# Optimization experiments

Measured on AMD Instinct MI355X. Metric: run time of the kernel, lower is better.

## Reference

```python
import jax, jax.numpy as jnp
import numpy as np

N_NODES = 50000
N_EDGES = 800000
IN_DIM = 64
HID_DIM = 64
OUT_DIM = 16
N_RELS = 16
N_BASES = 4


def setup_inputs() -> dict:
    key = jax.random.key(0)
    ks = jax.random.split(key, 11)
    feats = jax.random.normal(ks[0], (N_NODES, IN_DIM), dtype=jnp.float32)
    src = jax.random.randint(ks[1], (N_EDGES,), 0, N_NODES, dtype=jnp.int32)
    dst = jax.random.randint(ks[2], (N_EDGES,), 0, N_NODES, dtype=jnp.int32)
    edge_type = jax.random.randint(ks[3], (N_EDGES,), 0, N_RELS, dtype=jnp.int32)
    edge_norm = jax.random.uniform(ks[4], (N_EDGES,), dtype=jnp.float32)
    # basis-decomposed relation weights: W[r] = sum_b coef[r,b] * bases[b]
    bases1 = jax.random.normal(ks[5], (N_BASES, IN_DIM, HID_DIM), dtype=jnp.float32) * (1.0 / np.sqrt(IN_DIM))
    coef1 = jax.random.normal(ks[6], (N_RELS, N_BASES), dtype=jnp.float32)
    bias1 = jnp.zeros((HID_DIM,), dtype=jnp.float32)
    bases2 = jax.random.normal(ks[7], (N_BASES, HID_DIM, OUT_DIM), dtype=jnp.float32) * (1.0 / np.sqrt(HID_DIM))
    coef2 = jax.random.normal(ks[8], (N_RELS, N_BASES), dtype=jnp.float32)
    bias2 = jnp.zeros((OUT_DIM,), dtype=jnp.float32)
    return {"feats": feats, "src": src, "dst": dst, "edge_type": edge_type,
            "edge_norm": edge_norm, "bases1": bases1, "coef1": coef1, "bias1": bias1,
            "bases2": bases2, "coef2": coef2, "bias2": bias2}


def _rel_graph_conv(x, src, dst, edge_type, edge_norm, bases, coef, bias):
    """One RelGraphConv layer (basis decomposition, low-mem: gather coef, not W)."""
    xs = x[src]                                   # [E, in]  gather source feats
    t = jnp.einsum('ei,bio->ebo', xs, bases)      # [E, B, out] per-basis transform
    c = coef[edge_type]                            # [E, B]   per-edge relation coefs
    msg = jnp.einsum('eb,ebo->eo', c, t)          # [E, out]
    msg = msg * edge_norm[:, None]                # apply edge norm
    h = jax.ops.segment_sum(msg, dst, num_segments=N_NODES)  # scatter-add by dst
    return jax.nn.relu(h + bias)                  # bias + activation (dropout=0, eval)


def reference(feats, src, dst, edge_type, edge_norm, bases1, coef1, bias1, bases2, coef2, bias2):
    h = _rel_graph_conv(feats, src, dst, edge_type, edge_norm, bases1, coef1, bias1)
    h = _rel_graph_conv(h, src, dst, edge_type, edge_norm, bases2, coef2, bias2)
    return h
```

## Files before the change

### kernel.cpp

```cpp
#include <hip/hip_runtime.h>

#define N_NODES 50000
#define N_EDGES 800000

typedef __attribute__((ext_vector_type(8))) short bf16x8;
typedef __attribute__((ext_vector_type(4))) float f32x4;

__device__ __forceinline__ unsigned bf16rne(float x) {
  unsigned u = __float_as_uint(x);
  return (u + 0x7FFFu + ((u >> 16) & 1u)) >> 16;
}
__device__ __forceinline__ unsigned packbf2(float a, float b) {
  return bf16rne(a) | (bf16rne(b) << 16);
}
__device__ __forceinline__ float bflo(unsigned u) { return __uint_as_float(u << 16); }
__device__ __forceinline__ float bfhi(unsigned u) { return __uint_as_float(u & 0xFFFF0000u); }

__global__ __launch_bounds__(256) void k_prep_hist(
    const float4* __restrict__ feats4, uint2* __restrict__ xbf,
    const float* __restrict__ bases1, const float* __restrict__ bases2,
    unsigned short* __restrict__ b1T, unsigned short* __restrict__ b2p,
    const int* __restrict__ dst, int* __restrict__ deg,
    int* __restrict__ rank) {
  if (blockIdx.x < 3125) {
    const int i = blockIdx.x * 256 + threadIdx.x;
    float4 v = feats4[i];
    xbf[i] = make_uint2(packbf2(v.x, v.y), packbf2(v.z, v.w));
    rank[i] = atomicAdd(&deg[dst[i]], 1);
  } else {
    for (int idx = threadIdx.x; idx < 64 * 256; idx += 256) {
      int o = idx >> 8, q = idx & 255;
      b1T[idx] = (unsigned short)bf16rne(bases1[q * 64 + o]);
    }
    for (int idx = threadIdx.x; idx < 64 * 64; idx += 256) {
      int j = idx >> 6, k = idx & 63;
      int o = j >> 2, b = j & 3;
      b2p[idx] = (unsigned short)bf16rne(bases2[b * 1024 + k * 16 + o]);
    }
  }
}

__global__ __launch_bounds__(1024) void k_scan1(const int* __restrict__ deg,
                                                int* __restrict__ rowp,
                                                int* __restrict__ bsum) {
  __shared__ int wsum[16];
  const int tid = threadIdx.x, lane = tid & 63, wid = tid >> 6;
  const int i = blockIdx.x * 1024 + tid;
  int v = (i < N_NODES) ? deg[i] : 0;
  int incl = v;
#pragma unroll
  for (int off = 1; off < 64; off <<= 1) {
    int t = __shfl_up(incl, off, 64);
    if (lane >= off) incl += t;
  }
  if (lane == 63) wsum[wid] = incl;
  __syncthreads();
  if (tid < 16) {
    int wi = wsum[tid];
#pragma unroll
    for (int off = 1; off < 16; off <<= 1) {
      int t = __shfl_up(wi, off, 64);
      if (lane >= off) wi += t;
    }
    wsum[tid] = wi;
  }
  __syncthreads();
  int woff = (wid > 0) ? wsum[wid - 1] : 0;
  int incl_all = incl + woff;
  if (i < N_NODES) rowp[i + 1] = incl_all;
  if (tid == 1023) bsum[blockIdx.x] = incl_all;
}

__global__ __launch_bounds__(1024) void k_scan3(int* __restrict__ rowp,
                                                const int* __restrict__ bsum,
                                                int nblk) {
  __shared__ int s_off;
  const int tid = threadIdx.x;
  if (tid < 64) {
    int v = (tid < nblk && tid < blockIdx.x) ? bsum[tid] : 0;
#pragma unroll
    for (int off = 32; off >= 1; off >>= 1) v += __shfl_down(v, off, 64);
    if (tid == 0) s_off = v;
  }
  __syncthreads();
  const int i = blockIdx.x * 1024 + tid;
  if (i < N_NODES) rowp[i + 1] += s_off;
  if (i == 0) rowp[0] = 0;
}

__global__ __launch_bounds__(256) void k_scatter(
    const int* __restrict__ src, const int* __restrict__ dst,
    const int* __restrict__ ety, const float* __restrict__ enorm,
    const int* __restrict__ rowp, const int* __restrict__ rank,
    unsigned* __restrict__ s_edge) {
  int e = blockIdx.x * 256 + threadIdx.x;
  if (e >= N_EDGES) return;
  const int pos = rowp[dst[e]] + rank[e];
  unsigned nq = (unsigned)(enorm[e] * 4096.f + 0.5f);
  nq = nq > 4095u ? 4095u : nq;
  s_edge[pos] = (unsigned)src[e] | ((unsigned)ety[e] << 16) | (nq << 20);
}

#define NMSCALE (1.f / 4096.f)

#define ROWB 264
__device__ __forceinline__ void gather_node(
    const int* __restrict__ rowp, const unsigned* __restrict__ s_edge,
    const uint2* __restrict__ xv, const float4* __restrict__ coefLDS,
    unsigned short* __restrict__ uA,
    int node, int m, int lane) {
  const int eslot = lane >> 4, ch4 = lane & 15;
  const int beg = rowp[node], end = rowp[node + 1];
  float4 a0 = {0, 0, 0, 0}, a1 = {0, 0, 0, 0}, a2 = {0, 0, 0, 0}, a3 = {0, 0, 0, 0};
  int j = beg + eslot;
  unsigned rec0 = 0, rec1 = 0;
  uint2 xp = {0, 0};
  if (j < end) rec0 = s_edge[j];
  if (j + 4 < end) rec1 = s_edge[j + 4];
  if (j < end) xp = xv[(rec0 & 0xFFFF) * 16 + ch4];
  while (j < end) {
    unsigned rec2 = 0;
    uint2 xp1 = {0, 0};
    if (j + 8 < end) rec2 = s_edge[j + 8];
    if (j + 4 < end) xp1 = xv[(rec1 & 0xFFFF) * 16 + ch4];
    const float nm = (float)(rec0 >> 20) * NMSCALE;
    const float4 c = coefLDS[(rec0 >> 16) & 15];
    const float w0 = nm * c.x, w1 = nm * c.y, w2 = nm * c.z, w3 = nm * c.w;
    const float x0 = bflo(xp.x), x1 = bfhi(xp.x), x2 = bflo(xp.y), x3 = bfhi(xp.y);
    a0.x += w0 * x0; a0.y += w0 * x1; a0.z += w0 * x2; a0.w += w0 * x3;
    a1.x += w1 * x0; a1.y += w1 * x1; a1.z += w1 * x2; a1.w += w1 * x3;
    a2.x += w2 * x0; a2.y += w2 * x1; a2.z += w2 * x2; a2.w += w2 * x3;
    a3.x += w3 * x0; a3.y += w3 * x1; a3.z += w3 * x2; a3.w += w3 * x3;
    j += 4; rec0 = rec1; rec1 = rec2; xp = xp1;
  }
#define RED1(x) x += __shfl_down(x, 32, 64)
  RED1(a0.x); RED1(a0.y); RED1(a0.z); RED1(a0.w);
  RED1(a1.x); RED1(a1.y); RED1(a1.z); RED1(a1.w);
  RED1(a2.x); RED1(a2.y); RED1(a2.z); RED1(a2.w);
  RED1(a3.x); RED1(a3.y); RED1(a3.z); RED1(a3.w);
#undef RED1
  if (eslot < 2) {
    unsigned short* row = uA + (eslot * 16 + m) * ROWB + 4 * ch4;
    *(uint2*)(row + 0 * 64) = make_uint2(packbf2(a0.x, a0.y), packbf2(a0.z, a0.w));
    *(uint2*)(row + 1 * 64) = make_uint2(packbf2(a1.x, a1.y), packbf2(a1.z, a1.w));
    *(uint2*)(row + 2 * 64) = make_uint2(packbf2(a2.x, a2.y), packbf2(a2.z, a2.w));
    *(uint2*)(row + 3 * 64) = make_uint2(packbf2(a3.x, a3.y), packbf2(a3.z, a3.w));
  }
}

__global__ __launch_bounds__(256) void k_l1_fused(
    const int* __restrict__ rowp, const unsigned* __restrict__ s_edge,
    const uint2* __restrict__ xbf, const float* __restrict__ coef1,
    const unsigned short* __restrict__ b1T,
    const float* __restrict__ bias1,
    const unsigned short* __restrict__ b2p,
    uint2* __restrict__ y2bf) {
  __shared__ __align__(16) unsigned short uA[2 * 16 * ROWB];
  __shared__ float coefs[64];
  __shared__ float cmat[16 * 68];
  const int wid = threadIdx.x >> 6, lane = threadIdx.x & 63;
  if (threadIdx.x < 64) coefs[threadIdx.x] = coef1[threadIdx.x];
  __syncthreads();
  const int nbase = blockIdx.x * 16;
#pragma unroll
  for (int jn = 0; jn < 4; ++jn) {
    const int m = wid * 4 + jn;
    gather_node(rowp, s_edge, xbf, (const float4*)coefs, uA, nbase + m, m, lane);
  }
  __syncthreads();
  const int nloc = lane & 15, kgrp = lane >> 4;
  f32x4 acc1 = {0.f, 0.f, 0.f, 0.f};
#pragma unroll
  for (int ks = 0; ks < 8; ++ks) {
    const int k0 = ks * 32 + kgrp * 8;
    const bf16x8 b = *(const bf16x8*)&b1T[(wid * 16 + nloc) * 256 + k0];
    const bf16x8 aS0 = *(const bf16x8*)&uA[(0 * 16 + nloc) * ROWB + k0];
    acc1 = __builtin_amdgcn_mfma_f32_16x16x32_bf16(aS0, b, acc1, 0, 0, 0);
    const bf16x8 aS1 = *(const bf16x8*)&uA[(1 * 16 + nloc) * ROWB + k0];
    acc1 = __builtin_amdgcn_mfma_f32_16x16x32_bf16(aS1, b, acc1, 0, 0, 0);
  }
  {
    const int o = wid * 16 + nloc;
    const float bs = bias1[o];
#pragma unroll
    for (int r = 0; r < 4; ++r) {
      const int m = (lane >> 4) * 4 + r;
      cmat[m * 68 + o] = fmaxf(acc1[r] + bs, 0.f);
    }
  }
  __syncthreads();
  f32x4 acc2 = {0.f, 0.f, 0.f, 0.f};
#pragma unroll
  for (int ks = 0; ks < 2; ++ks) {
    const int k0 = ks * 32 + kgrp * 8;
    const float4 c0 = *(const float4*)&cmat[nloc * 68 + k0];
    const float4 c1 = *(const float4*)&cmat[nloc * 68 + k0 + 4];
    union { bf16x8 v; unsigned u[4]; } au;
    au.u[0] = packbf2(c0.x, c0.y); au.u[1] = packbf2(c0.z, c0.w);
    au.u[2] = packbf2(c1.x, c1.y); au.u[3] = packbf2(c1.z, c1.w);
    const bf16x8 b = *(const bf16x8*)&b2p[(wid * 16 + nloc) * 64 + k0];
    acc2 = __builtin_amdgcn_mfma_f32_16x16x32_bf16(au.v, b, acc2, 0, 0, 0);
  }
  __syncthreads();
#pragma unroll
  for (int r = 0; r < 4; ++r) {
    const int m = (lane >> 4) * 4 + r;
    cmat[m * 68 + wid * 16 + nloc] = acc2[r];
  }
  __syncthreads();
  const int nl = threadIdx.x >> 4, c4 = threadIdx.x & 15;
  const float* cr = &cmat[nl * 68 + 4 * c4];
  y2bf[(size_t)(nbase + nl) * 16 + c4] =
      make_uint2(packbf2(cr[0], cr[1]), packbf2(cr[2], cr[3]));
}

__global__ __launch_bounds__(256) void k_l2_gather(
    const int* __restrict__ rowp, const unsigned* __restrict__ s_edge,
    const uint4* __restrict__ y2v,
    const float* __restrict__ coef2, const float* __restrict__ bias2,
    float2* __restrict__ out) {
  __shared__ float coefs[64];
  if (threadIdx.x < 64) coefs[threadIdx.x] = coef2[threadIdx.x];
  __syncthreads();
  const float4* coefv = (const float4*)coefs;
  const int wid = threadIdx.x >> 6, lane = threadIdx.x & 63;
  const int eslot = lane >> 3, og = lane & 7;
  const int nbase = blockIdx.x * 8 + wid * 2;

  int j[2], jend[2];
  float a0[2] = {0.f, 0.f}, a1[2] = {0.f, 0.f};
  unsigned r0[2], r1[2];
  uint4 yp[2];
#pragma unroll
  for (int m = 0; m < 2; ++m) {
    const int node = nbase + m;
    const int beg = rowp[node];
    jend[m] = rowp[node + 1];
    j[m] = beg + eslot;
    r0[m] = 0; r1[m] = 0;
    yp[m] = make_uint4(0, 0, 0, 0);
    if (j[m] < jend[m]) r0[m] = s_edge[j[m]];
    if (j[m] + 8 < jend[m]) r1[m] = s_edge[j[m] + 8];
  }
#pragma unroll
  for (int m = 0; m < 2; ++m)
    if (j[m] < jend[m]) yp[m] = y2v[(r0[m] & 0xFFFF) * 8 + og];

  while ((j[0] < jend[0]) | (j[1] < jend[1])) {
#pragma unroll
    for (int m = 0; m < 2; ++m) {
      unsigned r2 = 0;
      uint4 yp1 = make_uint4(0, 0, 0, 0);
      if (j[m] + 16 < jend[m]) r2 = s_edge[j[m] + 16];
      if (j[m] + 8 < jend[m]) yp1 = y2v[(r1[m] & 0xFFFF) * 8 + og];
      if (j[m] < jend[m]) {
        const float nm = (float)(r0[m] >> 20) * NMSCALE;
        const float4 c = coefv[(r0[m] >> 16) & 15];
        a0[m] += nm * (c.x * bflo(yp[m].x) + c.y * bfhi(yp[m].x) +
                       c.z * bflo(yp[m].y) + c.w * bfhi(yp[m].y));
        a1[m] += nm * (c.x * bflo(yp[m].z) + c.y * bfhi(yp[m].z) +
                       c.z * bflo(yp[m].w) + c.w * bfhi(yp[m].w));
      }
      j[m] += 8; r0[m] = r1[m]; r1[m] = r2; yp[m] = yp1;
    }
  }
#pragma unroll
  for (int m = 0; m < 2; ++m) {
    a0[m] += __shfl_down(a0[m], 32, 64);
    a0[m] += __shfl_down(a0[m], 16, 64);
    a0[m] += __shfl_down(a0[m], 8, 64);
    a1[m] += __shfl_down(a1[m], 32, 64);
    a1[m] += __shfl_down(a1[m], 16, 64);
    a1[m] += __shfl_down(a1[m], 8, 64);
  }
  if (eslot == 0) {
    const float b0 = bias2[2 * og], b1 = bias2[2 * og + 1];
#pragma unroll
    for (int m = 0; m < 2; ++m) {
      out[(size_t)(nbase + m) * 8 + og] =
          make_float2(fmaxf(a0[m] + b0, 0.f), fmaxf(a1[m] + b1, 0.f));
    }
  }
}

extern "C" void kernel_launch(void* const* d_in, const int* in_sizes, int n_in,
                              void* d_out, int out_size, void* d_ws, size_t ws_size,
                              hipStream_t stream) {
  const float* feats  = (const float*)d_in[0];
  const int*   src    = (const int*)d_in[1];
  const int*   dst    = (const int*)d_in[2];
  const int*   etype  = (const int*)d_in[3];
  const float* enorm  = (const float*)d_in[4];
  const float* bases1 = (const float*)d_in[5];
  const float* coef1  = (const float*)d_in[6];
  const float* bias1  = (const float*)d_in[7];
  const float* bases2 = (const float*)d_in[8];
  const float* coef2  = (const float*)d_in[9];
  const float* bias2  = (const float*)d_in[10];

  uint2* xbf    = (uint2*)d_ws;
  uint2* y2bf   = xbf + (size_t)N_NODES * 16;
  unsigned* s_edge = (unsigned*)(y2bf + (size_t)N_NODES * 16);
  int*   rank   = (int*)(s_edge + N_EDGES);
  unsigned short* b1T = (unsigned short*)(rank + N_EDGES);
  unsigned short* b2p = b1T + 64 * 256;
  int*   deg    = (int*)(b2p + 64 * 64);
  int*   rowp   = deg + N_NODES;
  int*   bsum   = rowp + N_NODES + 1;

  const int SCAN_BLKS = (N_NODES + 1023) / 1024;

  hipMemsetAsync(deg, 0, N_NODES * sizeof(int), stream);

  k_prep_hist<<<3126, 256, 0, stream>>>((const float4*)feats, xbf, bases1,
                                        bases2, b1T, b2p, dst, deg, rank);
  k_scan1<<<SCAN_BLKS, 1024, 0, stream>>>(deg, rowp, bsum);
  k_scan3<<<SCAN_BLKS, 1024, 0, stream>>>(rowp, bsum, SCAN_BLKS);
  k_scatter<<<N_EDGES / 256, 256, 0, stream>>>(src, dst, etype, enorm,
                                               rowp, rank, s_edge);
  k_l1_fused<<<N_NODES / 16, 256, 0, stream>>>(rowp, s_edge, xbf, coef1,
                                               b1T, bias1, b2p, y2bf);
  k_l2_gather<<<N_NODES / 8, 256, 0, stream>>>(rowp, s_edge,
                                               (const uint4*)y2bf, coef2,
                                               bias2, (float2*)d_out);
}
```

Baseline: 199.4 us.

## Replace global-atomic degree histogram with per-block LDS histograms

Degree counting for the CSR build moves from global atomics into a new kernel. Each of 64 blocks builds a shared-memory histogram over its edge chunk in four passes of node ranges, then writes per-block counts as 16-bit values. The scan kernel turns these into per-block prefix offsets and node degrees, and the scatter kernel adds the block offset to the local rank. This removes contended global atomics and the memset, at the cost of an extra kernel, a 64×N_NODES short array that scan1 must read and rewrite, and a histogram kernel that uses only 64 blocks.

```diff
diff --git a/kernel.cpp b/kernel.cpp
--- a/kernel.cpp
+++ b/kernel.cpp
@@ -16,17 +16,14 @@
 __device__ __forceinline__ float bflo(unsigned u) { return __uint_as_float(u << 16); }
 __device__ __forceinline__ float bfhi(unsigned u) { return __uint_as_float(u & 0xFFFF0000u); }
 
-__global__ __launch_bounds__(256) void k_prep_hist(
+__global__ __launch_bounds__(256) void k_pack(
     const float4* __restrict__ feats4, uint2* __restrict__ xbf,
     const float* __restrict__ bases1, const float* __restrict__ bases2,
-    unsigned short* __restrict__ b1T, unsigned short* __restrict__ b2p,
-    const int* __restrict__ dst, int* __restrict__ deg,
-    int* __restrict__ rank) {
+    unsigned short* __restrict__ b1T, unsigned short* __restrict__ b2p) {
   if (blockIdx.x < 3125) {
     const int i = blockIdx.x * 256 + threadIdx.x;
     float4 v = feats4[i];
     xbf[i] = make_uint2(packbf2(v.x, v.y), packbf2(v.z, v.w));
-    rank[i] = atomicAdd(&deg[dst[i]], 1);
   } else {
     for (int idx = threadIdx.x; idx < 64 * 256; idx += 256) {
       int o = idx >> 8, q = idx & 255;
@@ -40,13 +37,55 @@
   }
 }
 
-__global__ __launch_bounds__(1024) void k_scan1(const int* __restrict__ deg,
-                                                int* __restrict__ rowp,
-                                                int* __restrict__ bsum) {
+#define G_HIST 64
+#define CHUNK (N_EDGES / G_HIST)
+#define HPASS 4
+#define HBINS (N_NODES / HPASS)
+
+__global__ __launch_bounds__(512) void k_hist(
+    const int* __restrict__ dst, int* __restrict__ rank,
+    unsigned short* __restrict__ bh) {
+  __shared__ int hist[HBINS];
+  const int e0 = blockIdx.x * CHUNK;
+  unsigned short* bhrow = bh + (size_t)blockIdx.x * N_NODES;
+#pragma unroll 1
+  for (int p = 0; p < HPASS; ++p) {
+    const int lo = p * HBINS;
+    for (int i = threadIdx.x; i < HBINS; i += 512) hist[i] = 0;
+    __syncthreads();
+    for (int i = threadIdx.x; i < CHUNK; i += 512) {
+      const int d = dst[e0 + i] - lo;
+      if ((unsigned)d < (unsigned)HBINS)
+        rank[e0 + i] = atomicAdd(&hist[d], 1);
+    }
+    __syncthreads();
+    for (int i = threadIdx.x; i < HBINS; i += 512)
+      bhrow[lo + i] = (unsigned short)hist[i];
+    __syncthreads();
+  }
+}
+
+__global__ __launch_bounds__(1024) void k_scan1(
+    unsigned short* __restrict__ bh, int* __restrict__ rowp,
+    int* __restrict__ bsum) {
   __shared__ int wsum[16];
   const int tid = threadIdx.x, lane = tid & 63, wid = tid >> 6;
   const int i = blockIdx.x * 1024 + tid;
-  int v = (i < N_NODES) ? deg[i] : 0;
+  int v = 0;
+  if (i < N_NODES) {
+    int c[G_HIST];
+#pragma unroll
+    for (int b = 0; b < G_HIST; ++b)
+      c[b] = (int)bh[(size_t)b * N_NODES + i];
+    int s = 0;
+#pragma unroll
+    for (int b = 0; b < G_HIST; ++b) {
+      const int t = c[b];
+      bh[(size_t)b * N_NODES + i] = (unsigned short)s;
+      s += t;
+    }
+    v = s;
+  }
   int incl = v;
 #pragma unroll
   for (int off = 1; off < 64; off <<= 1) {
@@ -92,10 +131,12 @@
     const int* __restrict__ src, const int* __restrict__ dst,
     const int* __restrict__ ety, const float* __restrict__ enorm,
     const int* __restrict__ rowp, const int* __restrict__ rank,
-    unsigned* __restrict__ s_edge) {
+    const unsigned short* __restrict__ bh, unsigned* __restrict__ s_edge) {
   int e = blockIdx.x * 256 + threadIdx.x;
   if (e >= N_EDGES) return;
-  const int pos = rowp[dst[e]] + rank[e];
+  const int d = dst[e];
+  const int b = e / CHUNK;
+  const int pos = rowp[d] + (int)bh[(size_t)b * N_NODES + d] + rank[e];
   unsigned nq = (unsigned)(enorm[e] * 4096.f + 0.5f);
   nq = nq > 4095u ? 4095u : nq;
   s_edge[pos] = (unsigned)src[e] | ((unsigned)ety[e] << 16) | (nq << 20);
@@ -302,22 +343,21 @@
   uint2* y2bf   = xbf + (size_t)N_NODES * 16;
   unsigned* s_edge = (unsigned*)(y2bf + (size_t)N_NODES * 16);
   int*   rank   = (int*)(s_edge + N_EDGES);
-  unsigned short* b1T = (unsigned short*)(rank + N_EDGES);
+  unsigned short* bh = (unsigned short*)(rank + N_EDGES);
+  unsigned short* b1T = bh + (size_t)G_HIST * N_NODES;
   unsigned short* b2p = b1T + 64 * 256;
-  int*   deg    = (int*)(b2p + 64 * 64);
-  int*   rowp   = deg + N_NODES;
+  int*   rowp   = (int*)(b2p + 64 * 64);
   int*   bsum   = rowp + N_NODES + 1;
 
   const int SCAN_BLKS = (N_NODES + 1023) / 1024;
 
-  hipMemsetAsync(deg, 0, N_NODES * sizeof(int), stream);
-
-  k_prep_hist<<<3126, 256, 0, stream>>>((const float4*)feats, xbf, bases1,
-                                        bases2, b1T, b2p, dst, deg, rank);
-  k_scan1<<<SCAN_BLKS, 1024, 0, stream>>>(deg, rowp, bsum);
+  k_pack<<<3126, 256, 0, stream>>>((const float4*)feats, xbf, bases1,
+                                   bases2, b1T, b2p);
+  k_hist<<<G_HIST, 512, 0, stream>>>(dst, rank, bh);
+  k_scan1<<<SCAN_BLKS, 1024, 0, stream>>>(bh, rowp, bsum);
   k_scan3<<<SCAN_BLKS, 1024, 0, stream>>>(rowp, bsum, SCAN_BLKS);
   k_scatter<<<N_EDGES / 256, 256, 0, stream>>>(src, dst, etype, enorm,
-                                               rowp, rank, s_edge);
+                                               rowp, rank, bh, s_edge);
   k_l1_fused<<<N_NODES / 16, 256, 0, stream>>>(rowp, s_edge, xbf, coef1,
                                                b1T, bias1, b2p, y2bf);
   k_l2_gather<<<N_NODES / 8, 256, 0, stream>>>(rowp, s_edge,
```

Measured after the change: 209.4 us. +5.1%, slower.
